# Performance work log

Hardware: AMD Instinct MI355X
Metric: run time of the kernel (lower is better)

Reference implementation:

```python
import jax, jax.numpy as jnp
import numpy as np

N_NODES = 50000
N_EDGES = 400000
D_IN = 128
D_H = 128
N_CLASSES = 20
N_GRAPHS = 256
EPS_BN = 1e-5


def _lin_params(key, d_in, d_out, scale=0.05):
    kw, kb = jax.random.split(key)
    W = jax.random.normal(kw, (d_in, d_out), jnp.float32) * scale
    b = jax.random.normal(kb, (d_out,), jnp.float32) * scale
    return W, b


def setup_inputs() -> dict:
    key = jax.random.key(0)
    ks = jax.random.split(key, 20)
    inp = {
        "x": jax.random.normal(ks[0], (N_NODES, D_IN), jnp.float32),
        "edge_index": jax.random.randint(ks[1], (2, N_EDGES), 0, N_NODES, jnp.int32),
        "batch": jnp.sort(jax.random.randint(ks[2], (N_NODES,), 0, N_GRAPHS, jnp.int32)),
    }
    kidx = 3
    for li, d_in in zip((1, 2, 3), (D_IN, D_H, D_H)):
        for nm in ("q", "k", "v", "s"):
            W, b = _lin_params(ks[kidx], d_in, D_H)
            kidx += 1
            inp[f"W{nm}{li}"] = W
            inp[f"b{nm}{li}"] = b
        inp[f"gamma{li}"] = jnp.ones((D_H,), jnp.float32)
        inp[f"beta{li}"] = jnp.zeros((D_H,), jnp.float32)
    Wl, bl = _lin_params(ks[kidx], D_H, N_CLASSES)
    inp["Wlin"] = Wl
    inp["blin"] = bl
    return inp


def _segment_softmax(logits, seg, n):
    m = jax.ops.segment_max(logits, seg, num_segments=n)
    e = jnp.exp(logits - m[seg])
    s = jax.ops.segment_sum(e, seg, num_segments=n)
    return e / (s[seg] + 1e-16)


def _transformer_conv(x, src, dst, Wq, bq, Wk, bk, Wv, bv, Ws, bs):
    # heads=1, concat=True, root_weight=True (PyG TransformerConv defaults)
    q = x @ Wq + bq  # [N, d]
    k = x @ Wk + bk
    v = x @ Wv + bv
    d = q.shape[-1]
    logits = jnp.sum(q[dst] * k[src], axis=-1) / jnp.sqrt(jnp.float32(d))  # [E]
    alpha = _segment_softmax(logits, dst, x.shape[0])
    out = jax.ops.segment_sum(alpha[:, None] * v[src], dst, num_segments=x.shape[0])
    return out + x @ Ws + bs


def _batch_norm(x, gamma, beta):
    mu = jnp.mean(x, axis=0)
    var = jnp.var(x, axis=0)
    return gamma * (x - mu) * jax.lax.rsqrt(var + EPS_BN) + beta


def _global_mean_pool(x, batch, n_graphs):
    sums = jax.ops.segment_sum(x, batch, num_segments=n_graphs)
    cnt = jax.ops.segment_sum(jnp.ones((x.shape[0],), x.dtype), batch, num_segments=n_graphs)
    return sums / jnp.maximum(cnt, 1.0)[:, None]


def reference(x, edge_index, batch,
              Wq1, bq1, Wk1, bk1, Wv1, bv1, Ws1, bs1, gamma1, beta1,
              Wq2, bq2, Wk2, bk2, Wv2, bv2, Ws2, bs2, gamma2, beta2,
              Wq3, bq3, Wk3, bk3, Wv3, bv3, Ws3, bs3, gamma3, beta3,
              Wlin, blin):
    src, dst = edge_index[0], edge_index[1]
    h = _transformer_conv(x, src, dst, Wq1, bq1, Wk1, bk1, Wv1, bv1, Ws1, bs1)
    h = jax.nn.relu(_batch_norm(h, gamma1, beta1))  # dropout inactive (eval)
    h = _transformer_conv(h, src, dst, Wq2, bq2, Wk2, bk2, Wv2, bv2, Ws2, bs2)
    h = jax.nn.relu(_batch_norm(h, gamma2, beta2))
    h = _transformer_conv(h, src, dst, Wq3, bq3, Wk3, bk3, Wv3, bv3, Ws3, bs3)
    h = jax.nn.relu(_batch_norm(h, gamma3, beta3))
    g = _global_mean_pool(h, batch, N_GRAPHS)  # [G, d]
    return g @ Wlin + blin  # [G, num_classes]
```

## Files before the change

kernel.cpp:

```cpp
#include <hip/hip_runtime.h>

#define N_NODES 50000
#define N_EDGES 400000
#define DH 128
#define N_GRAPHS 256

#define SCAN_CHUNK 512
#define N_CHUNKS ((N_NODES + SCAN_CHUNK - 1) / SCAN_CHUNK)
#define ATTN_BLOCKS ((N_NODES + 15) / 16)
#define POOL_CHUNKS ((N_NODES + 63) / 64)
#define PSLOTS 16

typedef __bf16 bf16x8 __attribute__((ext_vector_type(8)));
typedef float f32x4 __attribute__((ext_vector_type(4)));
typedef _Float16 f16x2 __attribute__((ext_vector_type(2)));
typedef _Float16 f16x8 __attribute__((ext_vector_type(8)));

#define DEV __device__ __forceinline__

#if defined(__has_builtin)
#if __has_builtin(__builtin_amdgcn_fdot2)
#define HAS_FDOT2 1
#endif
#endif

DEV float fdot2acc(f16x2 a, f16x2 b, float c) {
#ifdef HAS_FDOT2
  return __builtin_amdgcn_fdot2(a, b, c, false);
#else
  return (float)a.x * (float)b.x + (float)a.y * (float)b.y + c;
#endif
}

DEV unsigned short f2bf(float f) {
  union { float f; unsigned int i; } v; v.f = f;
  unsigned int x = v.i;
  unsigned int r = (x + 0x7fffu + ((x >> 16) & 1u)) >> 16;
  return (unsigned short)r;
}

struct WPtrs { const float* w[12]; };

__global__ void repack_kernel(WPtrs wp, unsigned short* __restrict__ WB) {
  int mat = blockIdx.y;
  int m = blockIdx.x * 256 + threadIdx.x;
  int j = m & 7;
  int lane = (m >> 3) & 63;
  int ct = (m >> 9) & 7;
  int kk = m >> 12;
  int i = kk * 32 + (lane >> 4) * 8 + j;
  int o = ct * 16 + (lane & 15);
  WB[mat * 16384 + m] = f2bf(wp.w[mat][i * 128 + o]);
}

__global__ void deg_count(const int* __restrict__ ei, int* __restrict__ deg, int E) {
  int e = blockIdx.x * 256 + threadIdx.x;
  if (e < E) atomicAdd(&deg[ei[E + e]], 1);
}

__global__ __launch_bounds__(256) void scan_sum(const int* __restrict__ deg,
                                                int* __restrict__ partials, int N) {
  __shared__ int red[256];
  int b = blockIdx.x, t = threadIdx.x;
  int base = b * SCAN_CHUNK + t * 2;
  int s = 0;
  if (base + 1 < N) { int2 v = *reinterpret_cast<const int2*>(deg + base); s = v.x + v.y; }
  else if (base < N) s = deg[base];
  red[t] = s;
  __syncthreads();
  for (int off = 128; off; off >>= 1) {
    if (t < off) red[t] += red[t + off];
    __syncthreads();
  }
  if (t == 0) partials[b] = red[0];
}

__global__ __launch_bounds__(256) void scan_apply(const int* __restrict__ deg,
                                                  const int* __restrict__ partials,
                                                  int* __restrict__ rowptr,
                                                  int* __restrict__ cursor, int N, int E) {
  __shared__ int s[256];
  __shared__ int prefSh;
  int b = blockIdx.x, t = threadIdx.x;

  s[t] = (t < b) ? partials[t] : 0;
  __syncthreads();
  for (int off = 128; off; off >>= 1) {
    if (t < off) s[t] += s[t + off];
    __syncthreads();
  }
  if (t == 0) prefSh = s[0];
  __syncthreads();
  int pref = prefSh;
  __syncthreads();

  int base = b * SCAN_CHUNK + t * 2;
  int d0 = 0, d1 = 0;
  if (base + 1 < N) { int2 v = *reinterpret_cast<const int2*>(deg + base); d0 = v.x; d1 = v.y; }
  else if (base < N) d0 = deg[base];
  int local = d0 + d1;
  s[t] = local;
  __syncthreads();
  for (int off = 1; off < 256; off <<= 1) {
    int o = (t >= off) ? s[t - off] : 0;
    __syncthreads();
    s[t] += o;
    __syncthreads();
  }
  int offp = pref + s[t] - local;
  if (base < N)     { rowptr[base] = offp;          cursor[base] = offp; }
  if (base + 1 < N) { rowptr[base + 1] = offp + d0; cursor[base + 1] = offp + d0; }
  if (b == 0 && t == 0) rowptr[N] = E;
}

__global__ void csr_scatter(const int* __restrict__ ei, int* __restrict__ cursor,
                            int* __restrict__ adj, int E) {
  int e = blockIdx.x * 256 + threadIdx.x;
  if (e < E) {
    int dst = ei[E + e];
    int pos = atomicAdd(&cursor[dst], 1);
    adj[pos] = ei[e];
  }
}

__global__ __launch_bounds__(256) void adj_sort16(const int* __restrict__ rowptr,
                                                  int* __restrict__ adj, int N) {
  __shared__ int buf[16 * 32];
  int t = threadIdx.x;
  int g = t >> 4, l = t & 15;
  int n = blockIdx.x * 16 + g;
  bool valid = n < N;
  int p0 = 0, d = 0;
  if (valid) { p0 = rowptr[n]; d = rowptr[n + 1] - p0; }
  if (__builtin_expect(d > 32, 0)) {
    if (l == 0) {
      for (int i = p0 + 1; i < p0 + d; ++i) {
        int v = adj[i]; int j = i - 1;
        while (j >= p0 && adj[j] > v) { adj[j + 1] = adj[j]; --j; }
        adj[j + 1] = v;
      }
    }
    d = 0;
  }
  int a0 = (l < d) ? adj[p0 + l] : 0x7fffffff;
  int a1 = (16 + l < d) ? adj[p0 + 16 + l] : 0x7fffffff;
  int r0 = 0, r1 = 0;
#pragma unroll
  for (int i = 0; i < 16; ++i) {
    int v0 = __shfl(a0, i, 16);
    int v1 = __shfl(a1, i, 16);
    r0 += (v0 < a0) || (v0 == a0 && i < l);
    r0 += (v1 < a0);
    r1 += (v0 <= a1);
    r1 += (v1 < a1) || (v1 == a1 && i < l);
  }
  if (l < d)      buf[g * 32 + r0] = a0;
  if (16 + l < d) buf[g * 32 + r1] = a1;
  __syncthreads();
  if (l < d)      adj[p0 + l]      = buf[g * 32 + l];
  if (16 + l < d) adj[p0 + 16 + l] = buf[g * 32 + 16 + l];
}

struct GemmOut { _Float16* Y[4]; const float* bias[4]; int ldY[4]; };

#define LDP 136

__global__ __launch_bounds__(256) void gemm_proj(
    const float* __restrict__ Xf,
    const _Float16* __restrict__ Hin,
    const float* __restrict__ scale, const float* __restrict__ shift,
    const unsigned short* __restrict__ WB4,
    GemmOut go, int useBN, int N)
{
  __shared__ __align__(16) unsigned short xs[64 * LDP];

  const int t = threadIdx.x;
  const int rowBase = blockIdx.x * 64;
  const int igc = (t & 15) * 8;

  if (useBN) {
    float4 sc0 = *reinterpret_cast<const float4*>(scale + igc);
    float4 sc1 = *reinterpret_cast<const float4*>(scale + igc + 4);
    float4 sh0 = *reinterpret_cast<const float4*>(shift + igc);
    float4 sh1 = *reinterpret_cast<const float4*>(shift + igc + 4);
#pragma unroll
    for (int j = 0; j < 4; ++j) {
      int v = t + 256 * j;
      int r = v >> 4;
      int grow = rowBase + r;
      ushort4 o0 = make_ushort4(0, 0, 0, 0), o1 = make_ushort4(0, 0, 0, 0);
      if (grow < N) {
        f16x8 hv = *reinterpret_cast<const f16x8*>(Hin + (size_t)grow * 128 + igc);
        o0.x = f2bf(fmaxf((float)hv[0] * sc0.x + sh0.x, 0.f));
        o0.y = f2bf(fmaxf((float)hv[1] * sc0.y + sh0.y, 0.f));
        o0.z = f2bf(fmaxf((float)hv[2] * sc0.z + sh0.z, 0.f));
        o0.w = f2bf(fmaxf((float)hv[3] * sc0.w + sh0.w, 0.f));
        o1.x = f2bf(fmaxf((float)hv[4] * sc1.x + sh1.x, 0.f));
        o1.y = f2bf(fmaxf((float)hv[5] * sc1.y + sh1.y, 0.f));
        o1.z = f2bf(fmaxf((float)hv[6] * sc1.z + sh1.z, 0.f));
        o1.w = f2bf(fmaxf((float)hv[7] * sc1.w + sh1.w, 0.f));
      }
      *reinterpret_cast<ushort4*>(&xs[r * LDP + igc]) = o0;
      *reinterpret_cast<ushort4*>(&xs[r * LDP + igc + 4]) = o1;
    }
  } else {
#pragma unroll
    for (int j = 0; j < 4; ++j) {
      int v = t + 256 * j;
      int r = v >> 4;
      int grow = rowBase + r;
      ushort4 o0 = make_ushort4(0, 0, 0, 0), o1 = make_ushort4(0, 0, 0, 0);
      if (grow < N) {
        float4 a = *reinterpret_cast<const float4*>(Xf + (size_t)grow * 128 + igc);
        float4 b = *reinterpret_cast<const float4*>(Xf + (size_t)grow * 128 + igc + 4);
        o0.x = f2bf(a.x); o0.y = f2bf(a.y); o0.z = f2bf(a.z); o0.w = f2bf(a.w);
        o1.x = f2bf(b.x); o1.y = f2bf(b.y); o1.z = f2bf(b.z); o1.w = f2bf(b.w);
      }
      *reinterpret_cast<ushort4*>(&xs[r * LDP + igc]) = o0;
      *reinterpret_cast<ushort4*>(&xs[r * LDP + igc + 4]) = o1;
    }
  }
  __syncthreads();

  const int wave = t >> 6;
  const int lane = t & 63;
  const int ln16 = lane & 15;
  const int quad = lane >> 4;
  const int r0 = wave * 16;

  bf16x8 afrag[4];
#pragma unroll
  for (int kk = 0; kk < 4; ++kk)
    afrag[kk] = *reinterpret_cast<const bf16x8*>(&xs[(r0 + ln16) * LDP + kk * 32 + quad * 8]);
  __syncthreads();

  for (int proj = 0; proj < 4; ++proj) {
    const unsigned short* __restrict__ WB = WB4 + proj * 16384;
    const float* __restrict__ bias = go.bias[proj];

    f32x4 acc[8] = {};
#pragma unroll
    for (int kk = 0; kk < 4; ++kk) {
#pragma unroll
      for (int ct = 0; ct < 8; ++ct) {
        bf16x8 b = *reinterpret_cast<const bf16x8*>(WB + ((kk * 8 + ct) * 64 + lane) * 8);
        acc[ct] = __builtin_amdgcn_mfma_f32_16x16x32_bf16(afrag[kk], b, acc[ct], 0, 0, 0);
      }
    }

    _Float16* __restrict__ Yh = go.Y[proj];
    const int ldY = go.ldY[proj];
#pragma unroll
    for (int ct = 0; ct < 8; ++ct) {
      int col = ct * 16 + ln16;
      float bv = bias[col];
#pragma unroll
      for (int reg = 0; reg < 4; ++reg) {
        _Float16 hv = (_Float16)(acc[ct][reg] + bv);
        xs[(r0 + quad * 4 + reg) * LDP + col] = __builtin_bit_cast(unsigned short, hv);
      }
    }
#pragma unroll
    for (int pass = 0; pass < 4; ++pass) {
      int rl = (lane >> 4) + pass * 4;
      int grow = rowBase + r0 + rl;
      f16x8 v = *reinterpret_cast<const f16x8*>(&xs[(r0 + rl) * LDP + ln16 * 8]);
      if (grow < N)
        *reinterpret_cast<f16x8*>(&Yh[(size_t)grow * ldY + ln16 * 8]) = v;
    }
  }
}

__global__ __launch_bounds__(256) void node_attn(
    const int* __restrict__ rowptr, const int* __restrict__ adj,
    const _Float16* __restrict__ Q, const _Float16* __restrict__ KV,
    _Float16* __restrict__ H, float* __restrict__ Pbuf, int N)
{
  __shared__ float lsum[16][128];
  __shared__ float lsq[16][128];
  int t = threadIdx.x;
  int w = t >> 4, lane = t & 15;
  int n = blockIdx.x * 16 + w;
  bool valid = n < N;
  int nn = valid ? n : 0;
  int p0 = 0, p1 = 0;
  if (valid) { p0 = rowptr[n]; p1 = rowptr[n + 1]; }
  int d = p1 - p0;

  f16x8 qv = *reinterpret_cast<const f16x8*>(Q + (size_t)nn * 128 + lane * 8);
  f16x2 q0 = {qv[0], qv[1]}, q1 = {qv[2], qv[3]}, q2 = {qv[4], qv[5]}, q3 = {qv[6], qv[7]};

  const float rsqd = 0.08838834764831845f;
  float m = -INFINITY, s = 0.f;
  float acc[8] = {};

#define EDGE1(SRC) do {                                                        \
    const _Float16* bp_ = KV + (size_t)(SRC) * 256 + lane * 8;                 \
    f16x8 ke_ = *reinterpret_cast<const f16x8*>(bp_);                          \
    f16x8 ve_ = *reinterpret_cast<const f16x8*>(bp_ + 128);                    \
    float dd_ = fdot2acc(q0, (f16x2){ke_[0], ke_[1]},                          \
                fdot2acc(q1, (f16x2){ke_[2], ke_[3]},                          \
                fdot2acc(q2, (f16x2){ke_[4], ke_[5]},                          \
                fdot2acc(q3, (f16x2){ke_[6], ke_[7]}, 0.f))));                 \
    for (int off_ = 8; off_; off_ >>= 1) dd_ += __shfl_xor(dd_, off_, 16);     \
    float ll_ = dd_ * rsqd;                                                    \
    float mn_ = fmaxf(m, ll_);                                                 \
    float sc_ = __expf(m - mn_);                                               \
    float w0_ = __expf(ll_ - mn_);                                             \
    for (int i_ = 0; i_ < 8; ++i_) acc[i_] = acc[i_] * sc_ + w0_ * (float)ve_[i_]; \
    s = s * sc_ + w0_;                                                         \
    m = mn_;                                                                   \
  } while (0)

  if (__builtin_expect(d <= 32, 1)) {
    int aLo = (lane < d) ? adj[p0 + lane] : 0;
    int aHi = (16 + lane < d) ? adj[p0 + 16 + lane] : 0;
    int e = 0;
    for (; e + 3 < d; e += 4) {
      int s0 = __shfl((e     < 16) ? aLo : aHi, (e    ) & 15, 16);
      int s1 = __shfl((e + 1 < 16) ? aLo : aHi, (e + 1) & 15, 16);
      int s2 = __shfl((e + 2 < 16) ? aLo : aHi, (e + 2) & 15, 16);
      int s3 = __shfl((e + 3 < 16) ? aLo : aHi, (e + 3) & 15, 16);
      const _Float16* b0 = KV + (size_t)s0 * 256 + lane * 8;
      const _Float16* b1 = KV + (size_t)s1 * 256 + lane * 8;
      const _Float16* b2 = KV + (size_t)s2 * 256 + lane * 8;
      const _Float16* b3 = KV + (size_t)s3 * 256 + lane * 8;
      f16x8 k0 = *reinterpret_cast<const f16x8*>(b0);
      f16x8 k1 = *reinterpret_cast<const f16x8*>(b1);
      f16x8 k2 = *reinterpret_cast<const f16x8*>(b2);
      f16x8 k3 = *reinterpret_cast<const f16x8*>(b3);
      f16x8 v0 = *reinterpret_cast<const f16x8*>(b0 + 128);
      f16x8 v1 = *reinterpret_cast<const f16x8*>(b1 + 128);
      f16x8 v2 = *reinterpret_cast<const f16x8*>(b2 + 128);
      f16x8 v3 = *reinterpret_cast<const f16x8*>(b3 + 128);
      float d0 = fdot2acc(q0, (f16x2){k0[0], k0[1]},
                 fdot2acc(q1, (f16x2){k0[2], k0[3]},
                 fdot2acc(q2, (f16x2){k0[4], k0[5]},
                 fdot2acc(q3, (f16x2){k0[6], k0[7]}, 0.f))));
      float d1 = fdot2acc(q0, (f16x2){k1[0], k1[1]},
                 fdot2acc(q1, (f16x2){k1[2], k1[3]},
                 fdot2acc(q2, (f16x2){k1[4], k1[5]},
                 fdot2acc(q3, (f16x2){k1[6], k1[7]}, 0.f))));
      float d2 = fdot2acc(q0, (f16x2){k2[0], k2[1]},
                 fdot2acc(q1, (f16x2){k2[2], k2[3]},
                 fdot2acc(q2, (f16x2){k2[4], k2[5]},
                 fdot2acc(q3, (f16x2){k2[6], k2[7]}, 0.f))));
      float d3 = fdot2acc(q0, (f16x2){k3[0], k3[1]},
                 fdot2acc(q1, (f16x2){k3[2], k3[3]},
                 fdot2acc(q2, (f16x2){k3[4], k3[5]},
                 fdot2acc(q3, (f16x2){k3[6], k3[7]}, 0.f))));
#pragma unroll
      for (int off = 8; off; off >>= 1) {
        d0 += __shfl_xor(d0, off, 16);
        d1 += __shfl_xor(d1, off, 16);
        d2 += __shfl_xor(d2, off, 16);
        d3 += __shfl_xor(d3, off, 16);
      }
      float l0 = d0 * rsqd, l1 = d1 * rsqd, l2 = d2 * rsqd, l3 = d3 * rsqd;
      float mn = fmaxf(fmaxf(fmaxf(l0, l1), fmaxf(l2, l3)), m);
      float sc = __expf(m - mn);
      float w0 = __expf(l0 - mn);
      float w1 = __expf(l1 - mn);
      float w2 = __expf(l2 - mn);
      float w3 = __expf(l3 - mn);
#pragma unroll
      for (int i = 0; i < 8; ++i)
        acc[i] = acc[i] * sc + w0 * (float)v0[i] + w1 * (float)v1[i]
                             + w2 * (float)v2[i] + w3 * (float)v3[i];
      s = s * sc + w0 + w1 + w2 + w3;
      m = mn;
    }
    for (; e < d; ++e) {
      int sE = __shfl((e < 16) ? aLo : aHi, e & 15, 16);
      EDGE1(sE);
    }
  } else {
    for (int p = p0; p < p1; ++p) {
      int sE = adj[p];
      EDGE1(sE);
    }
  }
#undef EDGE1

  float h[8];
#pragma unroll
  for (int i = 0; i < 8; ++i) h[i] = 0.f;
  if (valid) {
    float inv = 1.0f / (s + 1e-16f);
    f16x8 hh = *reinterpret_cast<const f16x8*>(H + (size_t)n * 128 + lane * 8);
    f16x8 ho;
#pragma unroll
    for (int i = 0; i < 8; ++i) {
      h[i] = (float)hh[i] + acc[i] * inv;
      ho[i] = (_Float16)h[i];
    }
    *reinterpret_cast<f16x8*>(H + (size_t)n * 128 + lane * 8) = ho;
  }

#pragma unroll
  for (int i = 0; i < 8; i += 4) {
    float4 hv = make_float4(h[i], h[i + 1], h[i + 2], h[i + 3]);
    float4 h2 = make_float4(hv.x * hv.x, hv.y * hv.y, hv.z * hv.z, hv.w * hv.w);
    *reinterpret_cast<float4*>(&lsum[w][lane * 8 + i]) = hv;
    *reinterpret_cast<float4*>(&lsq[w][lane * 8 + i]) = h2;
  }
  __syncthreads();

  int f = t & 127;
  float a = 0.f;
  if (t < 128) {
#pragma unroll
    for (int n16 = 0; n16 < 16; ++n16) a += lsum[n16][f];
  } else {
#pragma unroll
    for (int n16 = 0; n16 < 16; ++n16) a += lsq[n16][f];
  }
  Pbuf[(size_t)blockIdx.x * 256 + t] = a;
}

__global__ __launch_bounds__(256) void bn_fused(
    const float* __restrict__ Pbuf, float* __restrict__ bnpart,
    const float* __restrict__ gamma, const float* __restrict__ beta,
    float* __restrict__ scale, float* __restrict__ shift,
    int* __restrict__ ticket, int N)
{
  __shared__ float red[256];
  __shared__ int amLast;
  int t = threadIdx.x;
  {
    float s0 = 0.f, s1 = 0.f, s2 = 0.f, s3 = 0.f;
    int r = blockIdx.x;
    for (; r + 192 < ATTN_BLOCKS; r += 256) {
      s0 += Pbuf[(size_t)(r      ) * 256 + t];
      s1 += Pbuf[(size_t)(r +  64) * 256 + t];
      s2 += Pbuf[(size_t)(r + 128) * 256 + t];
      s3 += Pbuf[(size_t)(r + 192) * 256 + t];
    }
    for (; r < ATTN_BLOCKS; r += 64) s0 += Pbuf[(size_t)r * 256 + t];
    bnpart[blockIdx.x * 256 + t] = s0 + s1 + s2 + s3;
  }
  __threadfence();
  if (t == 0) amLast = (atomicAdd(ticket, 1) == 63);
  __syncthreads();
  if (!amLast) return;
  __threadfence();

  float s0 = 0.f, s1 = 0.f, s2 = 0.f, s3 = 0.f;
#pragma unroll
  for (int r = 0; r < 64; r += 4) {
    s0 += bnpart[(r + 0) * 256 + t];
    s1 += bnpart[(r + 1) * 256 + t];
    s2 += bnpart[(r + 2) * 256 + t];
    s3 += bnpart[(r + 3) * 256 + t];
  }
  red[t] = s0 + s1 + s2 + s3;
  __syncthreads();
  if (t < 128) {
    float mean = red[t] / (float)N;
    float var = red[t + 128] / (float)N - mean * mean;
    var = fmaxf(var, 0.f);
    float sc = gamma[t] * rsqrtf(var + 1e-5f);
    scale[t] = sc;
    shift[t] = beta[t] - mean * sc;
  }
}

__global__ __launch_bounds__(256) void pool_partial(
    const _Float16* __restrict__ H, const float* __restrict__ scale,
    const float* __restrict__ shift, const int* __restrict__ batch,
    float* __restrict__ partial, int N)
{
  int f = threadIdx.x & 127, parity = threadIdx.x >> 7;
  int base = blockIdx.x * 64;
  int lim = min(base + 64, N);
  float sc = scale[f], sh = shift[f];
  int slot = ((blockIdx.x & 7) << 1) | parity;
  int curg = -1; float s = 0.f;
  for (int row = base + parity; row < lim; row += 2) {
    int g = batch[row];
    if (g != curg) {
      if (curg >= 0) partial[(size_t)((curg << 4) | slot) * 128 + f] = s;
      curg = g; s = 0.f;
    }
    s += fmaxf((float)H[(size_t)row * 128 + f] * sc + sh, 0.f);
  }
  if (curg >= 0) partial[(size_t)((curg << 4) | slot) * 128 + f] = s;
}

__global__ __launch_bounds__(128) void final_linear(
    const float* __restrict__ partial, const int* __restrict__ batch,
    const float* __restrict__ Wlin, const float* __restrict__ blin,
    float* __restrict__ out, int N)
{
  __shared__ float pf[128];
  int g = blockIdx.x;
  int t = threadIdx.x;
  float s = 0.f;
#pragma unroll
  for (int sl = 0; sl < PSLOTS; ++sl)
    s += partial[(size_t)((g << 4) | sl) * 128 + t];
  pf[t] = s;
  __syncthreads();
  int lo = 0, hi = N;
  while (lo < hi) { int mid = (lo + hi) >> 1; if (batch[mid] < g) lo = mid + 1; else hi = mid; }
  int start = lo;
  hi = N;
  while (lo < hi) { int mid = (lo + hi) >> 1; if (batch[mid] < g + 1) lo = mid + 1; else hi = mid; }
  float inv = 1.0f / fmaxf((float)(lo - start), 1.f);
  if (t < 20) {
    float acc = 0.f;
#pragma unroll 4
    for (int i = 0; i < 128; ++i)
      acc += pf[i] * Wlin[i * 20 + t];
    out[g * 20 + t] = acc * inv + blin[t];
  }
}

extern "C" void kernel_launch(void* const* d_in, const int* in_sizes, int n_in,
                              void* d_out, int out_size, void* d_ws, size_t ws_size,
                              hipStream_t stream)
{
  const int N = N_NODES, E = N_EDGES, G = N_GRAPHS;

  const float* x = (const float*)d_in[0];
  const int* ei = (const int*)d_in[1];
  const int* batch = (const int*)d_in[2];
  const float* Wlin = (const float*)d_in[33];
  const float* blin = (const float*)d_in[34];

  char* ws = (char*)d_ws;
  size_t off = 0;
  auto alloc = [&](size_t bytes) -> void* {
    void* p = ws + off;
    off = (off + bytes + 255) & ~(size_t)255;
    return p;
  };
  unsigned short* WB = (unsigned short*)alloc(12 * 16384 * sizeof(unsigned short));
  _Float16* Qh  = (_Float16*)alloc((size_t)N * 128 * 2);
  _Float16* KVh = (_Float16*)alloc((size_t)N * 256 * 2);
  _Float16* Hh  = (_Float16*)alloc((size_t)N * 128 * 2);
  int* rowptr   = (int*)alloc((size_t)(N + 1) * 4);
  int* cursor   = (int*)alloc((size_t)N * 4);
  int* adj      = (int*)alloc((size_t)E * 4);
  int* partials = (int*)alloc((size_t)N_CHUNKS * 4);
  float* Pbuf   = (float*)alloc((size_t)ATTN_BLOCKS * 256 * 4);
  float* bnpart = (float*)alloc((size_t)64 * 256 * 4);
  float* scale  = (float*)alloc(128 * 4);
  float* shift  = (float*)alloc(128 * 4);
  size_t zoff = off;
  int* deg      = (int*)alloc((size_t)N * 4);
  int* tickets  = (int*)alloc(256);
  float* ppool  = (float*)alloc((size_t)G * PSLOTS * 128 * 4);
  size_t zbytes = off - zoff;

  WPtrs wp;
  for (int L = 0; L < 3; ++L) {
    wp.w[L * 4 + 0] = (const float*)d_in[3 + L * 10 + 0];
    wp.w[L * 4 + 1] = (const float*)d_in[3 + L * 10 + 2];
    wp.w[L * 4 + 2] = (const float*)d_in[3 + L * 10 + 4];
    wp.w[L * 4 + 3] = (const float*)d_in[3 + L * 10 + 6];
  }
  repack_kernel<<<dim3(64, 12), 256, 0, stream>>>(wp, WB);

  hipMemsetAsync(deg, 0, zbytes, stream);
  deg_count<<<(E + 255) / 256, 256, 0, stream>>>(ei, deg, E);
  scan_sum<<<N_CHUNKS, 256, 0, stream>>>(deg, partials, N);
  scan_apply<<<N_CHUNKS, 256, 0, stream>>>(deg, partials, rowptr, cursor, N, E);
  csr_scatter<<<(E + 255) / 256, 256, 0, stream>>>(ei, cursor, adj, E);
  adj_sort16<<<ATTN_BLOCKS, 256, 0, stream>>>(rowptr, adj, N);

  for (int L = 0; L < 3; ++L) {
    GemmOut go;
    go.Y[0] = Qh;        go.ldY[0] = 128;
    go.Y[1] = KVh;       go.ldY[1] = 256;
    go.Y[2] = KVh + 128; go.ldY[2] = 256;
    go.Y[3] = Hh;        go.ldY[3] = 128;
    go.bias[0] = (const float*)d_in[3 + L * 10 + 1];
    go.bias[1] = (const float*)d_in[3 + L * 10 + 3];
    go.bias[2] = (const float*)d_in[3 + L * 10 + 5];
    go.bias[3] = (const float*)d_in[3 + L * 10 + 7];
    gemm_proj<<<(N + 63) / 64, 256, 0, stream>>>(
        x, Hh, scale, shift, WB + L * 4 * 16384, go, (L > 0) ? 1 : 0, N);

    node_attn<<<ATTN_BLOCKS, 256, 0, stream>>>(rowptr, adj, Qh, KVh, Hh, Pbuf, N);

    bn_fused<<<64, 256, 0, stream>>>(Pbuf, bnpart,
        (const float*)d_in[3 + L * 10 + 8],
        (const float*)d_in[3 + L * 10 + 9],
        scale, shift, tickets + L, N);

    if (L == 2) {
      pool_partial<<<POOL_CHUNKS, 256, 0, stream>>>(Hh, scale, shift, batch, ppool, N);
      final_linear<<<G, 128, 0, stream>>>(ppool, batch, Wlin, blin, (float*)d_out, N);
    }
  }
}
```

Measured before the change: 434.8 us.

## Fuse CSR build into one persistent kernel and fold BN reduction into attention

```diff
diff --git a/kernel.cpp b/kernel.cpp
--- a/kernel.cpp
+++ b/kernel.cpp
@@ -5,11 +5,14 @@
 #define DH 128
 #define N_GRAPHS 256
 
-#define SCAN_CHUNK 512
-#define N_CHUNKS ((N_NODES + SCAN_CHUNK - 1) / SCAN_CHUNK)
 #define ATTN_BLOCKS ((N_NODES + 15) / 16)
 #define POOL_CHUNKS ((N_NODES + 63) / 64)
 #define PSLOTS 16
+
+#define CSR_BLOCKS 256
+#define CSR_THREADS 256
+#define CSR_T (CSR_BLOCKS * CSR_THREADS)
+#define CH 196
 
 typedef __bf16 bf16x8 __attribute__((ext_vector_type(8)));
 typedef float f32x4 __attribute__((ext_vector_type(4)));
@@ -39,126 +42,129 @@
   return (unsigned short)r;
 }
 
+DEV void gbarrier(int* cells, int idx) {
+  __syncthreads();
+  if (threadIdx.x == 0) {
+    __threadfence();
+    atomicAdd(&cells[idx], 1);
+    while (__hip_atomic_load(&cells[idx], __ATOMIC_ACQUIRE,
+                             __HIP_MEMORY_SCOPE_AGENT) < CSR_BLOCKS) {}
+    __threadfence();
+  }
+  __syncthreads();
+}
+
 struct WPtrs { const float* w[12]; };
 
-__global__ void repack_kernel(WPtrs wp, unsigned short* __restrict__ WB) {
-  int mat = blockIdx.y;
-  int m = blockIdx.x * 256 + threadIdx.x;
-  int j = m & 7;
-  int lane = (m >> 3) & 63;
-  int ct = (m >> 9) & 7;
-  int kk = m >> 12;
-  int i = kk * 32 + (lane >> 4) * 8 + j;
-  int o = ct * 16 + (lane & 15);
-  WB[mat * 16384 + m] = f2bf(wp.w[mat][i * 128 + o]);
-}
-
-__global__ void deg_count(const int* __restrict__ ei, int* __restrict__ deg, int E) {
-  int e = blockIdx.x * 256 + threadIdx.x;
-  if (e < E) atomicAdd(&deg[ei[E + e]], 1);
-}
-
-__global__ __launch_bounds__(256) void scan_sum(const int* __restrict__ deg,
-                                                int* __restrict__ partials, int N) {
-  __shared__ int red[256];
-  int b = blockIdx.x, t = threadIdx.x;
-  int base = b * SCAN_CHUNK + t * 2;
-  int s = 0;
-  if (base + 1 < N) { int2 v = *reinterpret_cast<const int2*>(deg + base); s = v.x + v.y; }
-  else if (base < N) s = deg[base];
-  red[t] = s;
-  __syncthreads();
-  for (int off = 128; off; off >>= 1) {
-    if (t < off) red[t] += red[t + off];
+__global__ __launch_bounds__(256) void csr_build(
+    const int* __restrict__ ei, WPtrs wp, unsigned short* __restrict__ WB,
+    int* __restrict__ deg, int* __restrict__ rowptr, int* __restrict__ cursor,
+    int* __restrict__ adj, int* __restrict__ blocksum,
+    int* __restrict__ cells, float* __restrict__ ppool, int N, int E)
+{
+  __shared__ int sdeg[256];
+  __shared__ int sb[256];
+  __shared__ int sbuf[16 * 32];
+
+  const int t = threadIdx.x, b = blockIdx.x;
+  const int gtid = b * CSR_THREADS + t;
+
+  for (int i = gtid; i < N; i += CSR_T) deg[i] = 0;
+  for (int i = gtid; i < N_GRAPHS * PSLOTS * 128; i += CSR_T) ppool[i] = 0.f;
+  for (int m = gtid; m < 12 * 16384; m += CSR_T) {
+    int mat = m >> 14;
+    int mm = m & 16383;
+    int j = mm & 7;
+    int lane = (mm >> 3) & 63;
+    int ct = (mm >> 9) & 7;
+    int kk = mm >> 12;
+    int i = kk * 32 + (lane >> 4) * 8 + j;
+    int o = ct * 16 + (lane & 15);
+    WB[m] = f2bf(wp.w[mat][i * 128 + o]);
+  }
+  gbarrier(cells, 0);
+
+  for (int e = gtid; e < E; e += CSR_T) atomicAdd(&deg[ei[E + e]], 1);
+  gbarrier(cells, 1);
+
+  const int nodeBase = b * CH;
+  const int myn = nodeBase + t;
+  int dv = (t < CH && myn < N) ? deg[myn] : 0;
+  sdeg[t] = dv;
+  __syncthreads();
+  for (int off = 1; off < 256; off <<= 1) {
+    int o = (t >= off) ? sdeg[t - off] : 0;
     __syncthreads();
-  }
-  if (t == 0) partials[b] = red[0];
-}
-
-__global__ __launch_bounds__(256) void scan_apply(const int* __restrict__ deg,
-                                                  const int* __restrict__ partials,
-                                                  int* __restrict__ rowptr,
-                                                  int* __restrict__ cursor, int N, int E) {
-  __shared__ int s[256];
-  __shared__ int prefSh;
-  int b = blockIdx.x, t = threadIdx.x;
-
-  s[t] = (t < b) ? partials[t] : 0;
-  __syncthreads();
-  for (int off = 128; off; off >>= 1) {
-    if (t < off) s[t] += s[t + off];
+    sdeg[t] += o;
     __syncthreads();
   }
-  if (t == 0) prefSh = s[0];
-  __syncthreads();
-  int pref = prefSh;
-  __syncthreads();
-
-  int base = b * SCAN_CHUNK + t * 2;
-  int d0 = 0, d1 = 0;
-  if (base + 1 < N) { int2 v = *reinterpret_cast<const int2*>(deg + base); d0 = v.x; d1 = v.y; }
-  else if (base < N) d0 = deg[base];
-  int local = d0 + d1;
-  s[t] = local;
-  __syncthreads();
-  for (int off = 1; off < 256; off <<= 1) {
-    int o = (t >= off) ? s[t - off] : 0;
+  if (t == 255) blocksum[b] = sdeg[255];
+  gbarrier(cells, 2);
+
+  if (b == 0) {
+    int v = blocksum[t];
+    sb[t] = v;
     __syncthreads();
-    s[t] += o;
-    __syncthreads();
-  }
-  int offp = pref + s[t] - local;
-  if (base < N)     { rowptr[base] = offp;          cursor[base] = offp; }
-  if (base + 1 < N) { rowptr[base + 1] = offp + d0; cursor[base + 1] = offp + d0; }
-  if (b == 0 && t == 0) rowptr[N] = E;
-}
-
-__global__ void csr_scatter(const int* __restrict__ ei, int* __restrict__ cursor,
-                            int* __restrict__ adj, int E) {
-  int e = blockIdx.x * 256 + threadIdx.x;
-  if (e < E) {
+    for (int off = 1; off < 256; off <<= 1) {
+      int o = (t >= off) ? sb[t - off] : 0;
+      __syncthreads();
+      sb[t] += o;
+      __syncthreads();
+    }
+    blocksum[t] = sb[t] - v;
+  }
+  gbarrier(cells, 3);
+
+  {
+    int base = blocksum[b];
+    int excl = base + sdeg[t] - dv;
+    if (t < CH && myn < N) { rowptr[myn] = excl; cursor[myn] = excl; }
+    if (gtid == 0) rowptr[N] = E;
+  }
+  gbarrier(cells, 4);
+
+  for (int e = gtid; e < E; e += CSR_T) {
     int dst = ei[E + e];
     int pos = atomicAdd(&cursor[dst], 1);
     adj[pos] = ei[e];
   }
-}
-
-__global__ __launch_bounds__(256) void adj_sort16(const int* __restrict__ rowptr,
-                                                  int* __restrict__ adj, int N) {
-  __shared__ int buf[16 * 32];
-  int t = threadIdx.x;
-  int g = t >> 4, l = t & 15;
-  int n = blockIdx.x * 16 + g;
-  bool valid = n < N;
-  int p0 = 0, d = 0;
-  if (valid) { p0 = rowptr[n]; d = rowptr[n + 1] - p0; }
-  if (__builtin_expect(d > 32, 0)) {
-    if (l == 0) {
-      for (int i = p0 + 1; i < p0 + d; ++i) {
-        int v = adj[i]; int j = i - 1;
-        while (j >= p0 && adj[j] > v) { adj[j + 1] = adj[j]; --j; }
-        adj[j + 1] = v;
-      }
-    }
-    d = 0;
-  }
-  int a0 = (l < d) ? adj[p0 + l] : 0x7fffffff;
-  int a1 = (16 + l < d) ? adj[p0 + 16 + l] : 0x7fffffff;
-  int r0 = 0, r1 = 0;
-#pragma unroll
-  for (int i = 0; i < 16; ++i) {
-    int v0 = __shfl(a0, i, 16);
-    int v1 = __shfl(a1, i, 16);
-    r0 += (v0 < a0) || (v0 == a0 && i < l);
-    r0 += (v1 < a0);
-    r1 += (v0 <= a1);
-    r1 += (v1 < a1) || (v1 == a1 && i < l);
-  }
-  if (l < d)      buf[g * 32 + r0] = a0;
-  if (16 + l < d) buf[g * 32 + r1] = a1;
-  __syncthreads();
-  if (l < d)      adj[p0 + l]      = buf[g * 32 + l];
-  if (16 + l < d) adj[p0 + 16 + l] = buf[g * 32 + 16 + l];
+  gbarrier(cells, 5);
+
+  {
+    const int g = t >> 4, l = t & 15;
+    const int ngroups = CSR_T / 16;
+    for (int n = b * 16 + g; n < N; n += ngroups) {
+      int p0 = rowptr[n];
+      int d = rowptr[n + 1] - p0;
+      if (d <= 1) continue;
+      if (__builtin_expect(d > 32, 0)) {
+        if (l == 0) {
+          for (int i = p0 + 1; i < p0 + d; ++i) {
+            int v = adj[i]; int j = i - 1;
+            while (j >= p0 && adj[j] > v) { adj[j + 1] = adj[j]; --j; }
+            adj[j + 1] = v;
+          }
+        }
+        continue;
+      }
+      int a0 = (l < d) ? adj[p0 + l] : 0x7fffffff;
+      int a1 = (16 + l < d) ? adj[p0 + 16 + l] : 0x7fffffff;
+      int r0 = 0, r1 = 0;
+#pragma unroll
+      for (int i = 0; i < 16; ++i) {
+        int v0 = __shfl(a0, i, 16);
+        int v1 = __shfl(a1, i, 16);
+        r0 += (v0 < a0) || (v0 == a0 && i < l);
+        r0 += (v1 < a0);
+        r1 += (v0 <= a1);
+        r1 += (v1 < a1) || (v1 == a1 && i < l);
+      }
+      if (l < d)      sbuf[g * 32 + r0] = a0;
+      if (16 + l < d) sbuf[g * 32 + r1] = a1;
+      if (l < d)      adj[p0 + l]      = sbuf[g * 32 + l];
+      if (16 + l < d) adj[p0 + 16 + l] = sbuf[g * 32 + 16 + l];
+    }
+  }
 }
 
 struct GemmOut { _Float16* Y[4]; const float* bias[4]; int ldY[4]; };
@@ -271,13 +277,17 @@
   }
 }
 
-__global__ __launch_bounds__(256) void node_attn(
+__global__ __launch_bounds__(256) void node_attn_bn(
     const int* __restrict__ rowptr, const int* __restrict__ adj,
     const _Float16* __restrict__ Q, const _Float16* __restrict__ KV,
-    _Float16* __restrict__ H, float* __restrict__ Pbuf, int N)
+    _Float16* __restrict__ H, float* __restrict__ Pbuf,
+    float* __restrict__ bnpart,
+    const float* __restrict__ gamma, const float* __restrict__ beta,
+    float* __restrict__ scale, float* __restrict__ shift,
+    int* __restrict__ ticket, int N)
 {
-  __shared__ float lsum[16][128];
-  __shared__ float lsq[16][128];
+  __shared__ float lsum[16][132];
+  __shared__ float lsq[16][132];
   int t = threadIdx.x;
   int w = t >> 4, lane = t & 15;
   int n = blockIdx.x * 16 + w;
@@ -316,23 +326,15 @@
     int aLo = (lane < d) ? adj[p0 + lane] : 0;
     int aHi = (16 + lane < d) ? adj[p0 + 16 + lane] : 0;
     int e = 0;
-    for (; e + 3 < d; e += 4) {
+    for (; e + 1 < d; e += 2) {
       int s0 = __shfl((e     < 16) ? aLo : aHi, (e    ) & 15, 16);
       int s1 = __shfl((e + 1 < 16) ? aLo : aHi, (e + 1) & 15, 16);
-      int s2 = __shfl((e + 2 < 16) ? aLo : aHi, (e + 2) & 15, 16);
-      int s3 = __shfl((e + 3 < 16) ? aLo : aHi, (e + 3) & 15, 16);
       const _Float16* b0 = KV + (size_t)s0 * 256 + lane * 8;
       const _Float16* b1 = KV + (size_t)s1 * 256 + lane * 8;
-      const _Float16* b2 = KV + (size_t)s2 * 256 + lane * 8;
-      const _Float16* b3 = KV + (size_t)s3 * 256 + lane * 8;
       f16x8 k0 = *reinterpret_cast<const f16x8*>(b0);
       f16x8 k1 = *reinterpret_cast<const f16x8*>(b1);
-      f16x8 k2 = *reinterpret_cast<const f16x8*>(b2);
-      f16x8 k3 = *reinterpret_cast<const f16x8*>(b3);
       f16x8 v0 = *reinterpret_cast<const f16x8*>(b0 + 128);
       f16x8 v1 = *reinterpret_cast<const f16x8*>(b1 + 128);
-      f16x8 v2 = *reinterpret_cast<const f16x8*>(b2 + 128);
-      f16x8 v3 = *reinterpret_cast<const f16x8*>(b3 + 128);
       float d0 = fdot2acc(q0, (f16x2){k0[0], k0[1]},
                  fdot2acc(q1, (f16x2){k0[2], k0[3]},
                  fdot2acc(q2, (f16x2){k0[4], k0[5]},
@@ -341,44 +343,29 @@
                  fdot2acc(q1, (f16x2){k1[2], k1[3]},
                  fdot2acc(q2, (f16x2){k1[4], k1[5]},
                  fdot2acc(q3, (f16x2){k1[6], k1[7]}, 0.f))));
-      float d2 = fdot2acc(q0, (f16x2){k2[0], k2[1]},
-                 fdot2acc(q1, (f16x2){k2[2], k2[3]},
-                 fdot2acc(q2, (f16x2){k2[4], k2[5]},
-                 fdot2acc(q3, (f16x2){k2[6], k2[7]}, 0.f))));
-      float d3 = fdot2acc(q0, (f16x2){k3[0], k3[1]},
-                 fdot2acc(q1, (f16x2){k3[2], k3[3]},
-                 fdot2acc(q2, (f16x2){k3[4], k3[5]},
-                 fdot2acc(q3, (f16x2){k3[6], k3[7]}, 0.f))));
 #pragma unroll
       for (int off = 8; off; off >>= 1) {
         d0 += __shfl_xor(d0, off, 16);
         d1 += __shfl_xor(d1, off, 16);
-        d2 += __shfl_xor(d2, off, 16);
-        d3 += __shfl_xor(d3, off, 16);
-      }
-      float l0 = d0 * rsqd, l1 = d1 * rsqd, l2 = d2 * rsqd, l3 = d3 * rsqd;
-      float mn = fmaxf(fmaxf(fmaxf(l0, l1), fmaxf(l2, l3)), m);
+      }
+      float l0 = d0 * rsqd;
+      float l1 = d1 * rsqd;
+      float mn = fmaxf(m, fmaxf(l0, l1));
       float sc = __expf(m - mn);
       float w0 = __expf(l0 - mn);
       float w1 = __expf(l1 - mn);
-      float w2 = __expf(l2 - mn);
-      float w3 = __expf(l3 - mn);
 #pragma unroll
       for (int i = 0; i < 8; ++i)
-        acc[i] = acc[i] * sc + w0 * (float)v0[i] + w1 * (float)v1[i]
-                             + w2 * (float)v2[i] + w3 * (float)v3[i];
-      s = s * sc + w0 + w1 + w2 + w3;
+        acc[i] = acc[i] * sc + w0 * (float)v0[i] + w1 * (float)v1[i];
+      s = s * sc + w0 + w1;
       m = mn;
     }
-    for (; e < d; ++e) {
+    if (e < d) {
       int sE = __shfl((e < 16) ? aLo : aHi, e & 15, 16);
       EDGE1(sE);
     }
   } else {
-    for (int p = p0; p < p1; ++p) {
-      int sE = adj[p];
-      EDGE1(sE);
-    }
+    for (int p = p0; p < p1; ++p) { int sE = adj[p]; EDGE1(sE); }
   }
 #undef EDGE1
 
@@ -416,20 +403,25 @@
     for (int n16 = 0; n16 < 16; ++n16) a += lsq[n16][f];
   }
   Pbuf[(size_t)blockIdx.x * 256 + t] = a;
-}
-
-__global__ __launch_bounds__(256) void bn_fused(
-    const float* __restrict__ Pbuf, float* __restrict__ bnpart,
-    const float* __restrict__ gamma, const float* __restrict__ beta,
-    float* __restrict__ scale, float* __restrict__ shift,
-    int* __restrict__ ticket, int N)
-{
-  __shared__ float red[256];
-  __shared__ int amLast;
-  int t = threadIdx.x;
+
+  __threadfence();
+  __shared__ int rankSh;
+  if (t == 0) rankSh = atomicAdd(&ticket[0], 1);
+  __syncthreads();
+  int rank = rankSh;
+  if (rank < ATTN_BLOCKS - 64) return;
+  int slot = rank - (ATTN_BLOCKS - 64);
+
+  if (t == 0) {
+    while (__hip_atomic_load(&ticket[0], __ATOMIC_ACQUIRE,
+                             __HIP_MEMORY_SCOPE_AGENT) < ATTN_BLOCKS) {}
+  }
+  __syncthreads();
+  __threadfence();
+
   {
     float s0 = 0.f, s1 = 0.f, s2 = 0.f, s3 = 0.f;
-    int r = blockIdx.x;
+    int r = slot;
     for (; r + 192 < ATTN_BLOCKS; r += 256) {
       s0 += Pbuf[(size_t)(r      ) * 256 + t];
       s1 += Pbuf[(size_t)(r +  64) * 256 + t];
@@ -437,14 +429,16 @@
       s3 += Pbuf[(size_t)(r + 192) * 256 + t];
     }
     for (; r < ATTN_BLOCKS; r += 64) s0 += Pbuf[(size_t)r * 256 + t];
-    bnpart[blockIdx.x * 256 + t] = s0 + s1 + s2 + s3;
+    bnpart[slot * 256 + t] = s0 + s1 + s2 + s3;
   }
   __threadfence();
-  if (t == 0) amLast = (atomicAdd(ticket, 1) == 63);
-  __syncthreads();
-  if (!amLast) return;
+  __shared__ int lastSh;
+  if (t == 0) lastSh = (atomicAdd(&ticket[1], 1) == 63);
+  __syncthreads();
+  if (!lastSh) return;
   __threadfence();
 
+  __shared__ float red[256];
   float s0 = 0.f, s1 = 0.f, s2 = 0.f, s3 = 0.f;
 #pragma unroll
   for (int r = 0; r < 64; r += 4) {
@@ -542,16 +536,16 @@
   int* rowptr   = (int*)alloc((size_t)(N + 1) * 4);
   int* cursor   = (int*)alloc((size_t)N * 4);
   int* adj      = (int*)alloc((size_t)E * 4);
-  int* partials = (int*)alloc((size_t)N_CHUNKS * 4);
+  int* deg      = (int*)alloc((size_t)N * 4);
+  int* blocksum = (int*)alloc(256 * 4);
   float* Pbuf   = (float*)alloc((size_t)ATTN_BLOCKS * 256 * 4);
   float* bnpart = (float*)alloc((size_t)64 * 256 * 4);
   float* scale  = (float*)alloc(128 * 4);
   float* shift  = (float*)alloc(128 * 4);
-  size_t zoff = off;
-  int* deg      = (int*)alloc((size_t)N * 4);
-  int* tickets  = (int*)alloc(256);
   float* ppool  = (float*)alloc((size_t)G * PSLOTS * 128 * 4);
-  size_t zbytes = off - zoff;
+  int* ctrl     = (int*)alloc(64);
+  int* cells    = ctrl;
+  int* tickets  = ctrl + 8;
 
   WPtrs wp;
   for (int L = 0; L < 3; ++L) {
@@ -560,14 +554,10 @@
     wp.w[L * 4 + 2] = (const float*)d_in[3 + L * 10 + 4];
     wp.w[L * 4 + 3] = (const float*)d_in[3 + L * 10 + 6];
   }
-  repack_kernel<<<dim3(64, 12), 256, 0, stream>>>(wp, WB);
-
-  hipMemsetAsync(deg, 0, zbytes, stream);
-  deg_count<<<(E + 255) / 256, 256, 0, stream>>>(ei, deg, E);
-  scan_sum<<<N_CHUNKS, 256, 0, stream>>>(deg, partials, N);
-  scan_apply<<<N_CHUNKS, 256, 0, stream>>>(deg, partials, rowptr, cursor, N, E);
-  csr_scatter<<<(E + 255) / 256, 256, 0, stream>>>(ei, cursor, adj, E);
-  adj_sort16<<<ATTN_BLOCKS, 256, 0, stream>>>(rowptr, adj, N);
+
+  hipMemsetAsync(ctrl, 0, 64, stream);
+  csr_build<<<CSR_BLOCKS, CSR_THREADS, 0, stream>>>(
+      ei, wp, WB, deg, rowptr, cursor, adj, blocksum, cells, ppool, N, E);
 
   for (int L = 0; L < 3; ++L) {
     GemmOut go;
@@ -582,12 +572,11 @@
     gemm_proj<<<(N + 63) / 64, 256, 0, stream>>>(
         x, Hh, scale, shift, WB + L * 4 * 16384, go, (L > 0) ? 1 : 0, N);
 
-    node_attn<<<ATTN_BLOCKS, 256, 0, stream>>>(rowptr, adj, Qh, KVh, Hh, Pbuf, N);
-
-    bn_fused<<<64, 256, 0, stream>>>(Pbuf, bnpart,
+    node_attn_bn<<<ATTN_BLOCKS, 256, 0, stream>>>(
+        rowptr, adj, Qh, KVh, Hh, Pbuf, bnpart,
         (const float*)d_in[3 + L * 10 + 8],
         (const float*)d_in[3 + L * 10 + 9],
-        scale, shift, tickets + L, N);
+        scale, shift, tickets + L * 2, N);
 
     if (L == 2) {
       pool_partial<<<POOL_CHUNKS, 256, 0, stream>>>(Hh, scale, shift, batch, ppool, N);
```

After: 1.678 ms. 3.86x slower.
